# Performance work log

Measured on AMD Instinct MI355X. Metric: run time of the kernel, lower is better.

Reference implementation:

```python
import jax, jax.numpy as jnp
import numpy as np

N_NODES = 50000
N_EDGES = 800000
D = 64


def setup_inputs() -> dict:
    key = jax.random.key(0)
    k = jax.random.split(key, 8)
    h = jax.random.normal(k[0], (N_NODES, D), dtype=jnp.float32)
    edge_src = jax.random.randint(k[1], (N_EDGES,), 0, N_NODES, dtype=jnp.int32)
    edge_dst = jax.random.randint(k[2], (N_EDGES,), 0, N_NODES, dtype=jnp.int32)
    # normalized adjacency weights (e.g. 1/deg style values in (0,1))
    edge_w = jax.random.uniform(k[3], (N_EDGES,), dtype=jnp.float32)
    W_self = jax.random.normal(k[4], (D, D), dtype=jnp.float32) / np.sqrt(D)
    b_self = jnp.zeros((D,), dtype=jnp.float32)
    W_neigh = jax.random.normal(k[5], (D, D), dtype=jnp.float32) / np.sqrt(D)
    b_neigh = jnp.zeros((D,), dtype=jnp.float32)
    return {
        "h": h,
        "edge_src": edge_src,
        "edge_dst": edge_dst,
        "edge_w": edge_w,
        "W_self": W_self,
        "b_self": b_self,
        "W_neigh": W_neigh,
        "b_neigh": b_neigh,
    }


def reference(h, edge_src, edge_dst, edge_w, W_self, b_self, W_neigh, b_neigh):
    # neigh = A_norm @ h : sparse COO matmul as weighted gather + segment-sum
    # messages: [E, D]
    msgs = edge_w[:, None] * h[edge_src]
    neigh = jax.ops.segment_sum(msgs, edge_dst, num_segments=N_NODES)  # [N, D]
    # out = lin_self(h) + lin_neigh(neigh), relu; dropout is a no-op in eval mode
    out = (h @ W_self.T + b_self) + (neigh @ W_neigh.T + b_neigh)
    return jax.nn.relu(out)
```

## Files before the change

### kernel.cpp

```cpp
#include <hip/hip_runtime.h>

#define N_NODES 50000
#define N_EDGES 800000
#define D 64

#define NPB 200
#define NB  250
#define CAP 4096
#define BT  512
#define EPT 8
#define CHUNK_E (BT * EPT)
#define NCHUNKS ((N_EDGES + CHUNK_E - 1) / CHUNK_E)
#define CONVB 256
#define CT  1024
#define GBLK 16

typedef unsigned short ushort_t;
typedef unsigned int   uint_t;
typedef __attribute__((ext_vector_type(8))) short   short8;
typedef __attribute__((ext_vector_type(4))) float   float4v;

__device__ __forceinline__ ushort_t f2b(float f) {
    uint_t u = __float_as_uint(f);
    return (ushort_t)((u + 0x7FFFu + ((u >> 16) & 1u)) >> 16);
}
__device__ __forceinline__ float b2f(ushort_t b) {
    return __uint_as_float((uint_t)b << 16);
}
__device__ __forceinline__ uint_t rne_hi16(uint_t u) {
    return (u + 0x7FFFu + ((u >> 16) & 1u)) & 0xFFFF0000u;
}
__device__ __forceinline__ float lane_bcast(float v, int l) {
    return __int_as_float(__builtin_amdgcn_readlane(__float_as_int(v), l));
}


__global__ __launch_bounds__(BT) void bin_h2b_kernel(
    const int* __restrict__ src, const int* __restrict__ dst,
    const float* __restrict__ w, int* __restrict__ cursor,
    int2* __restrict__ bedges,
    const float* __restrict__ h, ushort_t* __restrict__ hb)
{
    if (blockIdx.x >= NCHUNKS) {
        const int nb = gridDim.x - NCHUNKS;
        for (int i = (blockIdx.x - NCHUNKS) * BT + threadIdx.x;
             i < N_NODES * D / 4; i += nb * BT) {
            const float4 v = ((const float4*)h)[i];
            ushort4 o;
            o.x = f2b(v.x); o.y = f2b(v.y); o.z = f2b(v.z); o.w = f2b(v.w);
            ((ushort4*)hb)[i] = o;
        }
        return;
    }

    __shared__ int lh[NB];
    __shared__ int loff[NB];
    __shared__ int lcur[NB];
    __shared__ int gpos[NB];
    __shared__ int part[256];
    __shared__ int2 stage[CHUNK_E];
    __shared__ unsigned char sbk[CHUNK_E];

    const int t = threadIdx.x;
    for (int i = t; i < NB; i += BT) lh[i] = 0;
    __syncthreads();

    const int base = blockIdx.x * CHUNK_E;
    int   my_b[EPT];
    int   my_p[EPT];
    float my_w[EPT];
#pragma unroll
    for (int k = 0; k < EPT; ++k) {
        const int e = base + k * BT + t;
        if (e < N_EDGES) {
            const int d = dst[e];
            const int b = (unsigned)d / NPB;
            my_b[k] = b;
            my_p[k] = (src[e] << 8) | (d - b * NPB);
            my_w[k] = w[e];
            atomicAdd(&lh[b], 1);
        } else {
            my_b[k] = -1;
        }
    }
    __syncthreads();

    const int v = (t < NB) ? lh[t] : 0;
    if (t < 256) part[t] = v;
    __syncthreads();
    for (int off = 1; off < 256; off <<= 1) {
        int p = 0;
        if (t < 256 && t >= off) p = part[t - off];
        __syncthreads();
        if (t < 256) part[t] += p;
        __syncthreads();
    }
    if (t < NB) { loff[t] = part[t] - v; lcur[t] = part[t] - v; }
    __syncthreads();

#pragma unroll
    for (int k = 0; k < EPT; ++k) {
        if (my_b[k] >= 0) {
            const int p = atomicAdd(&lcur[my_b[k]], 1);
            stage[p] = make_int2(my_p[k], __float_as_int(my_w[k]));
            sbk[p] = (unsigned char)my_b[k];
        }
    }
    __syncthreads();

    if (t < NB && lh[t] > 0)
        gpos[t] = t * CAP + atomicAdd(&cursor[t], lh[t]);
    __syncthreads();

    const int tot = min(N_EDGES - base, CHUNK_E);
    for (int s = t; s < tot; s += BT) {
        const int b = sbk[s];
        bedges[gpos[b] + (s - loff[b])] = stage[s];
    }
}

__global__ __launch_bounds__(CT) void bucket_csr_kernel(
    const int* __restrict__ cursor, const int2* __restrict__ bedges,
    uint_t* __restrict__ pedges, int2* __restrict__ offs2)
{
    __shared__ int    lcur[NPB];
    __shared__ int    part[256];
    __shared__ uint_t stage[CAP];

    const int b   = blockIdx.x;
    const int t   = threadIdx.x;
    const int gb  = b * CAP;
    const int cnt = min(cursor[b], CAP);

    if (t < NPB) lcur[t] = 0;
    __syncthreads();
    for (int e = t; e < cnt; e += CT)
        atomicAdd(&lcur[bedges[gb + e].x & 255], 1);
    __syncthreads();

    const int v = (t < NPB) ? lcur[t] : 0;
    if (t < 256) part[t] = v;
    __syncthreads();
    for (int off = 1; off < 256; off <<= 1) {
        int p = 0;
        if (t < 256 && t >= off) p = part[t - off];
        __syncthreads();
        if (t < 256) part[t] += p;
        __syncthreads();
    }
    if (t < NPB) {
        const int ex = part[t] - v;
        lcur[t] = ex;
        offs2[b * NPB + t] = make_int2(gb + ex, gb + ex + v);
    }
    __syncthreads();

    for (int e = t; e < cnt; e += CT) {
        const int2 r = bedges[gb + e];
        const int p = atomicAdd(&lcur[r.x & 255], 1);
        stage[p] = (uint_t)(r.x >> 8) | rne_hi16((uint_t)r.y);
    }
    __syncthreads();
    for (int s = t; s < cnt; s += CT)
        pedges[gb + s] = stage[s];
}

__global__ __launch_bounds__(512) void gather_linear_kernel(
    const ushort_t* __restrict__ hb, const uint_t* __restrict__ pedges,
    const int2* __restrict__ offs2,
    const float* __restrict__ Ws, const float* __restrict__ bs,
    const float* __restrict__ Wn, const float* __restrict__ bn,
    float* __restrict__ out)
{
    __shared__ ushort_t nstage[GBLK * D];

    const int wave  = threadIdx.x >> 6;
    const int lane  = threadIdx.x & 63;
    const int node0 = blockIdx.x * GBLK;

#pragma unroll
    for (int jj = 0; jj < 2; ++jj) {
        const int j = wave * 2 + jj;
        const int node = node0 + j;
        if (node < N_NODES) {
            const int2 be = offs2[node];
            const int beg = be.x, end = be.y;
            float acc = 0.f;
            int e = beg;
            for (; e + 16 <= end; e += 16) {
                uint_t r[16];
                float  vv[16];
#pragma unroll
                for (int k = 0; k < 16; ++k) r[k] = pedges[e + k];
#pragma unroll
                for (int k = 0; k < 16; ++k)
                    vv[k] = b2f(hb[(size_t)(r[k] & 0xFFFFu) * D + lane]);
#pragma unroll
                for (int k = 0; k < 16; ++k)
                    acc = fmaf(__uint_as_float(r[k] & 0xFFFF0000u), vv[k], acc);
            }
            for (; e + 4 <= end; e += 4) {
                uint_t r[4];
                float  vv[4];
#pragma unroll
                for (int k = 0; k < 4; ++k) r[k] = pedges[e + k];
#pragma unroll
                for (int k = 0; k < 4; ++k)
                    vv[k] = b2f(hb[(size_t)(r[k] & 0xFFFFu) * D + lane]);
#pragma unroll
                for (int k = 0; k < 4; ++k)
                    acc = fmaf(__uint_as_float(r[k] & 0xFFFF0000u), vv[k], acc);
            }
            for (; e < end; ++e) {
                const uint_t r = pedges[e];
                acc = fmaf(__uint_as_float(r & 0xFFFF0000u),
                           b2f(hb[(size_t)(r & 0xFFFFu) * D + lane]), acc);
            }
            nstage[j * D + lane] = f2b(acc);
        }
    }
    __syncthreads();

    const int nt = wave;
    if (nt >= 4 || node0 >= N_NODES) return;
    const int row16 = lane & 15;
    const int quad  = lane >> 4;

    const size_t abase = (size_t)(node0 + row16) * D + quad * 8;
    const short8 ah0 = *(const short8*)(hb + abase);
    const short8 ah1 = *(const short8*)(hb + abase + 32);
    const ushort_t* sp = nstage + row16 * D + quad * 8;
    const short8 an0 = *(const short8*)sp;
    const short8 an1 = *(const short8*)(sp + 32);

    const int col = nt * 16 + row16;
    const float* wsr = Ws + (size_t)col * D + quad * 8;
    const float* wnr = Wn + (size_t)col * D + quad * 8;
    short8 bw[4];
#pragma unroll
    for (int f = 0; f < 4; ++f) {
        const float* p = (f < 2 ? wsr : wnr) + (f & 1) * 32;
        const float4 w0 = *(const float4*)p;
        const float4 w1 = *(const float4*)(p + 4);
        short8 bwv;
        bwv[0] = (short)f2b(w0.x); bwv[1] = (short)f2b(w0.y);
        bwv[2] = (short)f2b(w0.z); bwv[3] = (short)f2b(w0.w);
        bwv[4] = (short)f2b(w1.x); bwv[5] = (short)f2b(w1.y);
        bwv[6] = (short)f2b(w1.z); bwv[7] = (short)f2b(w1.w);
        bw[f] = bwv;
    }
    float4v acc = {0.f, 0.f, 0.f, 0.f};
    acc = __builtin_amdgcn_mfma_f32_16x16x32_bf16(ah0, bw[0], acc, 0, 0, 0);
    acc = __builtin_amdgcn_mfma_f32_16x16x32_bf16(ah1, bw[1], acc, 0, 0, 0);
    acc = __builtin_amdgcn_mfma_f32_16x16x32_bf16(an0, bw[2], acc, 0, 0, 0);
    acc = __builtin_amdgcn_mfma_f32_16x16x32_bf16(an1, bw[3], acc, 0, 0, 0);

    const float bias = bs[col] + bn[col];
#pragma unroll
    for (int r = 0; r < 4; ++r) {
        const int m = quad * 4 + r;
        out[(size_t)(node0 + m) * D + col] = fmaxf(acc[r] + bias, 0.f);
    }
}

__global__ __launch_bounds__(256) void sage_scatter(
    const float* __restrict__ h,
    const int* __restrict__ edge_src,
    const int* __restrict__ edge_dst,
    const float* __restrict__ edge_w,
    float* __restrict__ neigh)
{
    const long long tid = (long long)blockIdx.x * blockDim.x + threadIdx.x;
    const int e = (int)(tid >> 6);
    const int d = (int)(tid & 63);
    if (e >= N_EDGES) return;
    atomicAdd(&neigh[(long long)edge_dst[e] * D + d],
              edge_w[e] * h[(long long)edge_src[e] * D + d]);
}

__global__ __launch_bounds__(256, 2) void linear_f32_kernel(
    const float* __restrict__ h, const float* __restrict__ neigh,
    const float* __restrict__ Ws, const float* __restrict__ bs,
    const float* __restrict__ Wn, const float* __restrict__ bn,
    float* __restrict__ out)
{
    const int lane   = threadIdx.x & 63;
    const int gwave  = (blockIdx.x * blockDim.x + threadIdx.x) >> 6;
    const int nwaves = (gridDim.x * blockDim.x) >> 6;

    float Wsr[D], Wnr[D];
#pragma unroll
    for (int k = 0; k < D; k += 4) {
        const float4 a = *(const float4*)&Ws[(size_t)lane * D + k];
        const float4 b = *(const float4*)&Wn[(size_t)lane * D + k];
        Wsr[k] = a.x; Wsr[k+1] = a.y; Wsr[k+2] = a.z; Wsr[k+3] = a.w;
        Wnr[k] = b.x; Wnr[k+1] = b.y; Wnr[k+2] = b.z; Wnr[k+3] = b.w;
    }
    const float bias = bs[lane] + bn[lane];

    for (int n = gwave; n < N_NODES; n += nwaves) {
        const float hv = h[(size_t)n * D + lane];
        const float nv = neigh[(size_t)n * D + lane];
        float o = bias;
#pragma unroll
        for (int k = 0; k < D; ++k) {
            o = fmaf(lane_bcast(hv, k), Wsr[k], o);
            o = fmaf(lane_bcast(nv, k), Wnr[k], o);
        }
        out[(size_t)n * D + lane] = fmaxf(o, 0.f);
    }
}

extern "C" void kernel_launch(void* const* d_in, const int* in_sizes, int n_in,
                              void* d_out, int out_size, void* d_ws, size_t ws_size,
                              hipStream_t stream)
{
    const float* h        = (const float*)d_in[0];
    const int*   edge_src = (const int*)d_in[1];
    const int*   edge_dst = (const int*)d_in[2];
    const float* edge_w   = (const float*)d_in[3];
    const float* W_self   = (const float*)d_in[4];
    const float* b_self   = (const float*)d_in[5];
    const float* W_neigh  = (const float*)d_in[6];
    const float* b_neigh  = (const float*)d_in[7];
    float*       out      = (float*)d_out;

    int2*     bedges = (int2*)d_ws;
    uint_t*   pedges = (uint_t*)(bedges + (size_t)NB * CAP);
    int2*     offs2  = (int2*)(pedges + (size_t)NB * CAP);
    ushort_t* hb     = (ushort_t*)(offs2 + N_NODES);
    int*      cursor = (int*)(hb + (size_t)N_NODES * D);
    const size_t needed = (size_t)NB * CAP * 8 + (size_t)NB * CAP * 4
                        + (size_t)N_NODES * 8 + (size_t)N_NODES * D * 2 + NB * 4;

    if (ws_size >= needed) {
        hipMemsetAsync(cursor, 0, NB * sizeof(int), stream);
        bin_h2b_kernel<<<NCHUNKS + CONVB, BT, 0, stream>>>(
            edge_src, edge_dst, edge_w, cursor, bedges, h, hb);
        bucket_csr_kernel<<<NB, CT, 0, stream>>>(cursor, bedges, pedges, offs2);
        gather_linear_kernel<<<(N_NODES + GBLK - 1) / GBLK, 512, 0, stream>>>(
            hb, pedges, offs2, W_self, b_self, W_neigh, b_neigh, out);
    } else {
        float* neigh_fb = (float*)d_ws;
        hipMemsetAsync(neigh_fb, 0, (size_t)N_NODES * D * sizeof(float), stream);
        const long long total = (long long)N_EDGES * 64;
        sage_scatter<<<(int)((total + 255) / 256), 256, 0, stream>>>(
            h, edge_src, edge_dst, edge_w, neigh_fb);
        linear_f32_kernel<<<1024, 256, 0, stream>>>(h, neigh_fb, W_self, b_self,
                                                    W_neigh, b_neigh, out);
    }
}
```

Measured before the change: 143.3 us.

## Fuse bucket CSR build with gather and linear into one per-bucket kernel

Merges the per-bucket CSR sort kernel and the gather+MFMA linear kernel into a single kernel. Each block keeps its sorted packed edges and offsets in shared memory, then has its 16 waves gather neighbour rows and run the bf16 MFMA for its 200 nodes. This removes the global pedges/offs2 round trip and one launch. In exchange, only 250 blocks of 1024 threads run the gather phase, compared with over 3000 smaller blocks before, so parallelism and latency hiding for the random hb gathers drop and shared-memory use per block rises.

```diff
diff --git a/kernel.cpp b/kernel.cpp
--- a/kernel.cpp
+++ b/kernel.cpp
@@ -13,7 +13,7 @@
 #define NCHUNKS ((N_EDGES + CHUNK_E - 1) / CHUNK_E)
 #define CONVB 256
 #define CT  1024
-#define GBLK 16
+#define NTILE ((NPB + 15) / 16)
 
 typedef unsigned short ushort_t;
 typedef unsigned int   uint_t;
@@ -119,13 +119,18 @@
     }
 }
 
-__global__ __launch_bounds__(CT) void bucket_csr_kernel(
+__global__ __launch_bounds__(CT) void csr_gather_kernel(
     const int* __restrict__ cursor, const int2* __restrict__ bedges,
-    uint_t* __restrict__ pedges, int2* __restrict__ offs2)
-{
-    __shared__ int    lcur[NPB];
-    __shared__ int    part[256];
-    __shared__ uint_t stage[CAP];
+    const ushort_t* __restrict__ hb,
+    const float* __restrict__ Ws, const float* __restrict__ bs,
+    const float* __restrict__ Wn, const float* __restrict__ bn,
+    float* __restrict__ out)
+{
+    __shared__ int      offs[NPB + 1];
+    __shared__ int      lcur[NPB];
+    __shared__ int      part[256];
+    __shared__ __align__(16) uint_t   stage[CAP];
+    __shared__ __align__(16) ushort_t nstage[NTILE * 16 * D];
 
     const int b   = blockIdx.x;
     const int t   = threadIdx.x;
@@ -150,9 +155,11 @@
     }
     if (t < NPB) {
         const int ex = part[t] - v;
+        offs[t] = ex;
         lcur[t] = ex;
-        offs2[b * NPB + t] = make_int2(gb + ex, gb + ex + v);
-    }
+    }
+    if (t == 0) offs[NPB] = cnt;
+    if (t < (NTILE * 16 - NPB) * D) nstage[NPB * D + t] = 0;
     __syncthreads();
 
     for (int e = t; e < cnt; e += CT) {
@@ -161,105 +168,81 @@
         stage[p] = (uint_t)(r.x >> 8) | rne_hi16((uint_t)r.y);
     }
     __syncthreads();
-    for (int s = t; s < cnt; s += CT)
-        pedges[gb + s] = stage[s];
-}
-
-__global__ __launch_bounds__(512) void gather_linear_kernel(
-    const ushort_t* __restrict__ hb, const uint_t* __restrict__ pedges,
-    const int2* __restrict__ offs2,
-    const float* __restrict__ Ws, const float* __restrict__ bs,
-    const float* __restrict__ Wn, const float* __restrict__ bn,
-    float* __restrict__ out)
-{
-    __shared__ ushort_t nstage[GBLK * D];
-
-    const int wave  = threadIdx.x >> 6;
-    const int lane  = threadIdx.x & 63;
-    const int node0 = blockIdx.x * GBLK;
-
-#pragma unroll
-    for (int jj = 0; jj < 2; ++jj) {
-        const int j = wave * 2 + jj;
-        const int node = node0 + j;
-        if (node < N_NODES) {
-            const int2 be = offs2[node];
-            const int beg = be.x, end = be.y;
-            float acc = 0.f;
-            int e = beg;
-            for (; e + 16 <= end; e += 16) {
-                uint_t r[16];
-                float  vv[16];
-#pragma unroll
-                for (int k = 0; k < 16; ++k) r[k] = pedges[e + k];
-#pragma unroll
-                for (int k = 0; k < 16; ++k)
-                    vv[k] = b2f(hb[(size_t)(r[k] & 0xFFFFu) * D + lane]);
-#pragma unroll
-                for (int k = 0; k < 16; ++k)
-                    acc = fmaf(__uint_as_float(r[k] & 0xFFFF0000u), vv[k], acc);
-            }
-            for (; e + 4 <= end; e += 4) {
-                uint_t r[4];
-                float  vv[4];
-#pragma unroll
-                for (int k = 0; k < 4; ++k) r[k] = pedges[e + k];
-#pragma unroll
-                for (int k = 0; k < 4; ++k)
-                    vv[k] = b2f(hb[(size_t)(r[k] & 0xFFFFu) * D + lane]);
-#pragma unroll
-                for (int k = 0; k < 4; ++k)
-                    acc = fmaf(__uint_as_float(r[k] & 0xFFFF0000u), vv[k], acc);
-            }
-            for (; e < end; ++e) {
-                const uint_t r = pedges[e];
-                acc = fmaf(__uint_as_float(r & 0xFFFF0000u),
-                           b2f(hb[(size_t)(r & 0xFFFFu) * D + lane]), acc);
-            }
-            nstage[j * D + lane] = f2b(acc);
-        }
-    }
-    __syncthreads();
-
-    const int nt = wave;
-    if (nt >= 4 || node0 >= N_NODES) return;
-    const int row16 = lane & 15;
-    const int quad  = lane >> 4;
-
-    const size_t abase = (size_t)(node0 + row16) * D + quad * 8;
-    const short8 ah0 = *(const short8*)(hb + abase);
-    const short8 ah1 = *(const short8*)(hb + abase + 32);
-    const ushort_t* sp = nstage + row16 * D + quad * 8;
-    const short8 an0 = *(const short8*)sp;
-    const short8 an1 = *(const short8*)(sp + 32);
-
-    const int col = nt * 16 + row16;
-    const float* wsr = Ws + (size_t)col * D + quad * 8;
-    const float* wnr = Wn + (size_t)col * D + quad * 8;
-    short8 bw[4];
-#pragma unroll
-    for (int f = 0; f < 4; ++f) {
-        const float* p = (f < 2 ? wsr : wnr) + (f & 1) * 32;
-        const float4 w0 = *(const float4*)p;
-        const float4 w1 = *(const float4*)(p + 4);
-        short8 bwv;
-        bwv[0] = (short)f2b(w0.x); bwv[1] = (short)f2b(w0.y);
-        bwv[2] = (short)f2b(w0.z); bwv[3] = (short)f2b(w0.w);
-        bwv[4] = (short)f2b(w1.x); bwv[5] = (short)f2b(w1.y);
-        bwv[6] = (short)f2b(w1.z); bwv[7] = (short)f2b(w1.w);
-        bw[f] = bwv;
-    }
-    float4v acc = {0.f, 0.f, 0.f, 0.f};
-    acc = __builtin_amdgcn_mfma_f32_16x16x32_bf16(ah0, bw[0], acc, 0, 0, 0);
-    acc = __builtin_amdgcn_mfma_f32_16x16x32_bf16(ah1, bw[1], acc, 0, 0, 0);
-    acc = __builtin_amdgcn_mfma_f32_16x16x32_bf16(an0, bw[2], acc, 0, 0, 0);
-    acc = __builtin_amdgcn_mfma_f32_16x16x32_bf16(an1, bw[3], acc, 0, 0, 0);
-
-    const float bias = bs[col] + bn[col];
-#pragma unroll
-    for (int r = 0; r < 4; ++r) {
-        const int m = quad * 4 + r;
-        out[(size_t)(node0 + m) * D + col] = fmaxf(acc[r] + bias, 0.f);
+
+    const int wave = t >> 6;
+    const int lane = t & 63;
+    const int nbeg = wave * 12 + min(wave, 8);
+    const int ncnt = 12 + (wave < 8 ? 1 : 0);
+    for (int ni = 0; ni < ncnt; ++ni) {
+        const int n   = nbeg + ni;
+        const int beg = offs[n], end = offs[n + 1];
+        float acc = 0.f;
+        int e = beg;
+        for (; e + 8 <= end; e += 8) {
+            uint_t r[8];
+            float  vv[8];
+#pragma unroll
+            for (int k = 0; k < 8; ++k) r[k] = stage[e + k];
+#pragma unroll
+            for (int k = 0; k < 8; ++k)
+                vv[k] = b2f(hb[(size_t)(r[k] & 0xFFFFu) * D + lane]);
+#pragma unroll
+            for (int k = 0; k < 8; ++k)
+                acc = fmaf(__uint_as_float(r[k] & 0xFFFF0000u), vv[k], acc);
+        }
+        for (; e < end; ++e) {
+            const uint_t r = stage[e];
+            acc = fmaf(__uint_as_float(r & 0xFFFF0000u),
+                       b2f(hb[(size_t)(r & 0xFFFFu) * D + lane]), acc);
+        }
+        nstage[n * D + lane] = f2b(acc);
+    }
+    __syncthreads();
+
+    const int node0b = b * NPB;
+    const int row16  = lane & 15;
+    const int quad   = lane >> 4;
+    for (int task = wave; task < NTILE * 4; task += 16) {
+        const int m  = task >> 2;
+        const int nt = task & 3;
+        const int arow = m * 16 + row16;
+
+        const size_t abase = (size_t)(node0b + arow) * D + quad * 8;
+        const short8 ah0 = *(const short8*)(hb + abase);
+        const short8 ah1 = *(const short8*)(hb + abase + 32);
+        const ushort_t* sp = nstage + arow * D + quad * 8;
+        const short8 an0 = *(const short8*)sp;
+        const short8 an1 = *(const short8*)(sp + 32);
+
+        const int col = nt * 16 + row16;
+        const float* wsr = Ws + (size_t)col * D + quad * 8;
+        const float* wnr = Wn + (size_t)col * D + quad * 8;
+        short8 bw[4];
+#pragma unroll
+        for (int f = 0; f < 4; ++f) {
+            const float* p = (f < 2 ? wsr : wnr) + (f & 1) * 32;
+            const float4 w0 = *(const float4*)p;
+            const float4 w1 = *(const float4*)(p + 4);
+            short8 bwv;
+            bwv[0] = (short)f2b(w0.x); bwv[1] = (short)f2b(w0.y);
+            bwv[2] = (short)f2b(w0.z); bwv[3] = (short)f2b(w0.w);
+            bwv[4] = (short)f2b(w1.x); bwv[5] = (short)f2b(w1.y);
+            bwv[6] = (short)f2b(w1.z); bwv[7] = (short)f2b(w1.w);
+            bw[f] = bwv;
+        }
+        float4v acc = {0.f, 0.f, 0.f, 0.f};
+        acc = __builtin_amdgcn_mfma_f32_16x16x32_bf16(ah0, bw[0], acc, 0, 0, 0);
+        acc = __builtin_amdgcn_mfma_f32_16x16x32_bf16(ah1, bw[1], acc, 0, 0, 0);
+        acc = __builtin_amdgcn_mfma_f32_16x16x32_bf16(an0, bw[2], acc, 0, 0, 0);
+        acc = __builtin_amdgcn_mfma_f32_16x16x32_bf16(an1, bw[3], acc, 0, 0, 0);
+
+        const float bias = bs[col] + bn[col];
+#pragma unroll
+        for (int r = 0; r < 4; ++r) {
+            const int mr = m * 16 + quad * 4 + r;
+            if (mr < NPB)
+                out[(size_t)(node0b + mr) * D + col] = fmaxf(acc[r] + bias, 0.f);
+        }
     }
 }
 
@@ -326,20 +309,16 @@
     float*       out      = (float*)d_out;
 
     int2*     bedges = (int2*)d_ws;
-    uint_t*   pedges = (uint_t*)(bedges + (size_t)NB * CAP);
-    int2*     offs2  = (int2*)(pedges + (size_t)NB * CAP);
-    ushort_t* hb     = (ushort_t*)(offs2 + N_NODES);
+    ushort_t* hb     = (ushort_t*)(bedges + (size_t)NB * CAP);
     int*      cursor = (int*)(hb + (size_t)N_NODES * D);
-    const size_t needed = (size_t)NB * CAP * 8 + (size_t)NB * CAP * 4
-                        + (size_t)N_NODES * 8 + (size_t)N_NODES * D * 2 + NB * 4;
+    const size_t needed = (size_t)NB * CAP * 8 + (size_t)N_NODES * D * 2 + NB * 4;
 
     if (ws_size >= needed) {
         hipMemsetAsync(cursor, 0, NB * sizeof(int), stream);
         bin_h2b_kernel<<<NCHUNKS + CONVB, BT, 0, stream>>>(
             edge_src, edge_dst, edge_w, cursor, bedges, h, hb);
-        bucket_csr_kernel<<<NB, CT, 0, stream>>>(cursor, bedges, pedges, offs2);
-        gather_linear_kernel<<<(N_NODES + GBLK - 1) / GBLK, 512, 0, stream>>>(
-            hb, pedges, offs2, W_self, b_self, W_neigh, b_neigh, out);
+        csr_gather_kernel<<<NB, CT, 0, stream>>>(
+            cursor, bedges, hb, W_self, b_self, W_neigh, b_neigh, out);
     } else {
         float* neigh_fb = (float*)d_ws;
         hipMemsetAsync(neigh_fb, 0, (size_t)N_NODES * D * sizeof(float), stream);
```

New measurement: 142.2 us. No clear change (-0.8%).
